# Kernel tuning notes

Measured on AMD Instinct MI355X. Metric: run time of the kernel, lower is better.

Reference implementation:

```python
import jax, jax.numpy as jnp
import numpy as np

HEADS = 16
DIM = 1024


def setup_inputs() -> dict:
    key = jax.random.key(0)
    ks = jax.random.split(key, 9)
    b, n, d = 2, 2048, DIM
    scale = 1.0 / np.sqrt(d)  # xavier-ish scale for weights
    x = jax.random.normal(ks[0], (b, n, d), dtype=jnp.float32)
    Wq = jax.random.normal(ks[1], (d, d), dtype=jnp.float32) * scale
    Wk = jax.random.normal(ks[2], (d, d), dtype=jnp.float32) * scale
    Wv = jax.random.normal(ks[3], (d, d), dtype=jnp.float32) * scale
    Wo = jax.random.normal(ks[4], (d, d), dtype=jnp.float32) * scale
    bq = jnp.zeros((d,), jnp.float32)
    bk = jnp.zeros((d,), jnp.float32)
    bv = jnp.zeros((d,), jnp.float32)
    bo = jnp.zeros((d,), jnp.float32)
    return {"x": x, "Wq": Wq, "bq": bq, "Wk": Wk, "bk": bk,
            "Wv": Wv, "bv": bv, "Wo": Wo, "bo": bo}


def reference(x, Wq, bq, Wk, bk, Wv, bv, Wo, bo):
    b, n, d = x.shape
    h = HEADS
    hd = d // h
    # torch Linear: y = x @ W.T + b  (W stored [out, in]; here square so W given as [d,d])
    q = x @ Wq.T + bq
    k = x @ Wk.T + bk
    v = x @ Wv.T + bv
    # b n (h d) -> b h n d
    q = q.reshape(b, n, h, hd).transpose(0, 2, 1, 3)
    k = k.reshape(b, n, h, hd).transpose(0, 2, 1, 3)
    v = v.reshape(b, n, h, hd).transpose(0, 2, 1, 3)
    # NOTE: scale is 1/sqrt(dim), not 1/sqrt(head_dim), faithful to source.
    scores = jnp.einsum('bhqd,bhkd->bhqk', q, k) / jnp.sqrt(jnp.float32(d))
    attn = jax.nn.softmax(scores, axis=-1)
    out = jnp.einsum('bhqk,bhkd->bhqd', attn, v)
    out = out.transpose(0, 2, 1, 3).reshape(b, n, d)  # b h n d -> b n (h d)
    return out @ Wo.T + bo
```

## Files before the change

### kernel.cpp

```cpp
#include <hip/hip_runtime.h>

typedef unsigned short u16t;
typedef __attribute__((ext_vector_type(8))) short bf16x8;
typedef __attribute__((ext_vector_type(4))) float f32x4;

#define DM   1024
#define SEQL 2048
#define NHD  16
#define HDD  64

#define GLL16(g, l) __builtin_amdgcn_global_load_lds( \
    (const __attribute__((address_space(1))) void*)(g), \
    (__attribute__((address_space(3))) void*)(l), 16, 0, 0)

__device__ __forceinline__ u16t f2bf(float f) {
  unsigned u = __float_as_uint(f);
  return (u16t)((u + 0x7fffu + ((u >> 16) & 1u)) >> 16);
}
__device__ __forceinline__ unsigned pack_bf16_2(float a, float b) {
  const unsigned ua = __float_as_uint(a) + 0x8000u;
  const unsigned ub = __float_as_uint(b) + 0x8000u;
  return __builtin_amdgcn_perm(ub, ua, 0x07060302);
}

struct ConvArgs { const float* src[5]; u16t* dst[5]; };

__global__ __launch_bounds__(256) void conv_kernel(ConvArgs a) {
  const int gid = blockIdx.x * 256 + threadIdx.x;
  const int e = gid << 2;
  int sel, off;
  if (e < 4194304) { sel = 0; off = e; }
  else { const int r = e - 4194304; sel = 1 + (r >> 20); off = r & 1048575; }
  const float4 f = *(const float4*)(a.src[sel] + off);
  union { u16t s[4]; uint2 u; } o;
  o.s[0] = f2bf(f.x); o.s[1] = f2bf(f.y); o.s[2] = f2bf(f.z); o.s[3] = f2bf(f.w);
  *(uint2*)(a.dst[sel] + off) = o.u;
}

__device__ __forceinline__ int gslot(int m, int kc) { return (m << 2) + (kc ^ ((m >> 1) & 3)); }

template<int MODE>
__device__ __forceinline__ void qkv_body(
    const u16t* __restrict__ X, const u16t* __restrict__ W,
    const float* __restrict__ bias, float oscale, u16t* __restrict__ outB,
    u16t* As, u16t* Bs, u16t* Es)
{
  const int tid = threadIdx.x;
  const int l = tid & 63, w = tid >> 6, q = l >> 4, ln = l & 15;
  const int trow0 = blockIdx.y << 7;
  const int dcol0 = blockIdx.x << 7;
  const int wm = (w >> 1) << 6, wn = (w & 1) << 6;

  const int s0 = (w << 6) + l, s1 = s0 + 256;
  const int m0 = s0 >> 2, kc0 = (s0 & 3) ^ ((m0 >> 1) & 3);
  const int m1 = s1 >> 2, kc1 = (s1 & 3) ^ ((m1 >> 1) & 3);
  const u16t* gA0 = X + (size_t)(trow0 + m0) * DM + (kc0 << 3);
  const u16t* gA1 = X + (size_t)(trow0 + m1) * DM + (kc1 << 3);
  const u16t* gB0 = W + (size_t)(dcol0 + m0) * DM + (kc0 << 3);
  const u16t* gB1 = W + (size_t)(dcol0 + m1) * DM + (kc1 << 3);
  u16t* const lA0 = &As[(w << 6) << 3];
  u16t* const lA1 = &As[((w << 6) + 256) << 3];
  u16t* const lB0 = &Bs[(w << 6) << 3];
  u16t* const lB1 = &Bs[((w << 6) + 256) << 3];

  f32x4 acc[4][4] = {};

  for (int kt = 0; kt < DM; kt += 32) {
    __syncthreads();
    GLL16(gA0 + kt, lA0);
    GLL16(gA1 + kt, lA1);
    GLL16(gB0 + kt, lB0);
    GLL16(gB1 + kt, lB1);
    __syncthreads();

    bf16x8 af[4], bfr[4];
    #pragma unroll
    for (int mi = 0; mi < 4; ++mi) {
      const int r = wm + (mi << 4) + ln;
      af[mi] = *(const bf16x8*)&((MODE == 1 ? Bs : As)[gslot(r, q) << 3]);
    }
    #pragma unroll
    for (int ni = 0; ni < 4; ++ni) {
      const int r = wn + (ni << 4) + ln;
      bfr[ni] = *(const bf16x8*)&((MODE == 1 ? As : Bs)[gslot(r, q) << 3]);
    }
    #pragma unroll
    for (int mi = 0; mi < 4; ++mi)
      #pragma unroll
      for (int ni = 0; ni < 4; ++ni)
        acc[mi][ni] = __builtin_amdgcn_mfma_f32_16x16x32_bf16(af[mi], bfr[ni], acc[mi][ni], 0, 0, 0);
  }

  __syncthreads();

  if (MODE == 1) {
    #pragma unroll
    for (int mi = 0; mi < 4; ++mi) {
      const int dl = wm + (mi << 4) + (q << 2);
      const float4 b4 = *(const float4*)&bias[dcol0 + dl];
      #pragma unroll
      for (int ni = 0; ni < 4; ++ni) {
        const int tl = wn + (ni << 4) + ln;
        uint2 pk;
        pk.x = pack_bf16_2((acc[mi][ni][0] + b4.x) * oscale, (acc[mi][ni][1] + b4.y) * oscale);
        pk.y = pack_bf16_2((acc[mi][ni][2] + b4.z) * oscale, (acc[mi][ni][3] + b4.w) * oscale);
        *(uint2*)&Es[tl * 136 + dl] = pk;
      }
    }
    __syncthreads();
    #pragma unroll
    for (int it = 0; it < 8; ++it) {
      const int u = (it << 8) + tid;
      const int tl = u >> 4, c8 = u & 15;
      const uint4 vv = *(const uint4*)&Es[tl * 136 + (c8 << 3)];
      const int tok = trow0 + tl;
      const int b = tok >> 11, n = tok & (SEQL - 1);
      const int dg = dcol0 + (c8 << 3);
      const int h = dg >> 6, hd = dg & 63;
      *(uint4*)&outB[((size_t)(b * NHD + h) * SEQL + n) * HDD + hd] = vv;
    }
  } else {
    #pragma unroll
    for (int ni = 0; ni < 4; ++ni) {
      const int dl = wn + (ni << 4) + ln;
      const float bv = bias[dcol0 + dl];
      #pragma unroll
      for (int mi = 0; mi < 4; ++mi) {
        const int g = (wm >> 2) + (mi << 2) + q;
        const int g6 = g & 15;
        const int gp = (g & 16) | (g6 & 8) | ((g6 & 3) << 1) | ((g6 >> 2) & 1);
        uint2 pk;
        pk.x = pack_bf16_2(acc[mi][ni][0] + bv, acc[mi][ni][1] + bv);
        pk.y = pack_bf16_2(acc[mi][ni][2] + bv, acc[mi][ni][3] + bv);
        *(uint2*)&Es[dl * 136 + (gp << 2)] = pk;
      }
    }
    __syncthreads();
    #pragma unroll
    for (int it = 0; it < 8; ++it) {
      const int u = (it << 8) + tid;
      const int dl = u >> 4, c8 = u & 15;
      const uint4 vv = *(const uint4*)&Es[dl * 136 + (c8 << 3)];
      const int dg = dcol0 + dl;
      const int h = dg >> 6, hd = dg & 63;
      const int b = trow0 >> 11;
      const int n = (trow0 & (SEQL - 1)) + (c8 << 3);
      *(uint4*)&outB[((size_t)(b * NHD + h) * HDD + hd) * SEQL + n] = vv;
    }
  }
}

struct QKVArgs { const u16t* W[3]; const float* b[3]; u16t* dst[3]; };

__global__ __launch_bounds__(256) void qkv_kernel(const u16t* __restrict__ X, QKVArgs g) {
  __shared__ alignas(16) u16t smem[17408];
  u16t* As = smem;
  u16t* Bs = smem + 4096;
  u16t* Es = smem;
  const int z = blockIdx.z;
  if (z == 2)      qkv_body<2>(X, g.W[2], g.b[2], 1.0f, g.dst[2], As, Bs, Es);
  else if (z == 1) qkv_body<1>(X, g.W[1], g.b[1], 1.0f, g.dst[1], As, Bs, Es);
  else             qkv_body<1>(X, g.W[0], g.b[0], 0.03125f, g.dst[0], As, Bs, Es);
}

__global__ __launch_bounds__(256) void outproj_kernel(
    const u16t* __restrict__ A, const u16t* __restrict__ W,
    const float* __restrict__ bias, float* __restrict__ outF)
{
  __shared__ alignas(16) u16t As[128 * 32];
  __shared__ alignas(16) u16t Bs[128 * 32];

  const int tid = threadIdx.x;
  const int l = tid & 63, w = tid >> 6, q = l >> 4, ln = l & 15;
  const int row0 = blockIdx.y << 7;
  const int col0 = blockIdx.x << 7;
  const int wm = (w >> 1) << 6, wn = (w & 1) << 6;

  const int s0 = (w << 6) + l, s1 = s0 + 256;
  const int m0 = s0 >> 2, kc0 = (s0 & 3) ^ ((m0 >> 1) & 3);
  const int m1 = s1 >> 2, kc1 = (s1 & 3) ^ ((m1 >> 1) & 3);
  const u16t* gA0 = A + (size_t)(row0 + m0) * DM + (kc0 << 3);
  const u16t* gA1 = A + (size_t)(row0 + m1) * DM + (kc1 << 3);
  const u16t* gB0 = W + (size_t)(col0 + m0) * DM + (kc0 << 3);
  const u16t* gB1 = W + (size_t)(col0 + m1) * DM + (kc1 << 3);
  u16t* const lA0 = &As[(w << 6) << 3];
  u16t* const lA1 = &As[((w << 6) + 256) << 3];
  u16t* const lB0 = &Bs[(w << 6) << 3];
  u16t* const lB1 = &Bs[((w << 6) + 256) << 3];

  f32x4 acc[4][4] = {};

  for (int kt = 0; kt < DM; kt += 32) {
    __syncthreads();
    GLL16(gA0 + kt, lA0);
    GLL16(gA1 + kt, lA1);
    GLL16(gB0 + kt, lB0);
    GLL16(gB1 + kt, lB1);
    __syncthreads();

    bf16x8 af[4], bfr[4];
    #pragma unroll
    for (int mi = 0; mi < 4; ++mi)
      af[mi] = *(const bf16x8*)&As[gslot(wm + (mi << 4) + ln, q) << 3];
    #pragma unroll
    for (int ni = 0; ni < 4; ++ni)
      bfr[ni] = *(const bf16x8*)&Bs[gslot(wn + (ni << 4) + ln, q) << 3];
    #pragma unroll
    for (int mi = 0; mi < 4; ++mi)
      #pragma unroll
      for (int ni = 0; ni < 4; ++ni)
        acc[mi][ni] = __builtin_amdgcn_mfma_f32_16x16x32_bf16(af[mi], bfr[ni], acc[mi][ni], 0, 0, 0);
  }

  #pragma unroll
  for (int ni = 0; ni < 4; ++ni) {
    const int col = col0 + wn + (ni << 4) + ln;
    const float bv = bias[col];
    #pragma unroll
    for (int mi = 0; mi < 4; ++mi)
      #pragma unroll
      for (int r = 0; r < 4; ++r) {
        const int row = row0 + wm + (mi << 4) + (q << 2) + r;
        outF[(size_t)row * DM + col] = acc[mi][ni][r] + bv;
      }
  }
}

__global__ __launch_bounds__(256) void attn_kernel(
    const u16t* __restrict__ Qb, const u16t* __restrict__ Kb,
    const u16t* __restrict__ Vt, u16t* __restrict__ ctx)
{
  __shared__ alignas(16) u16t smem[17408];
  u16t* Qs = smem;
  u16t* Os = smem;
  u16t* Ks = smem + 9216;
  u16t* Vs = smem + 13312;

  const int tid = threadIdx.x;
  const int l = tid & 63, w = tid >> 6;
  const int q = l >> 4, ln = l & 15;
  const int bh = blockIdx.y, q0 = blockIdx.x << 7;
  const size_t hb = (size_t)bh * SEQL * HDD;
  const u16t* Qg = Qb + hb;
  const u16t* Kg = Kb + hb;
  const u16t* Vg = Vt + hb;

  #pragma unroll
  for (int i = 0; i < 4; ++i) {
    const int u = (i << 8) + tid;
    const int r = u >> 3, c = (u & 7) ^ (r & 7);
    GLL16(Qg + (size_t)(q0 + r) * HDD + (c << 3), &Qs[((i << 8) + (w << 6)) << 3]);
  }

  f32x4 accO[2][4] = {};
  float lsum[2] = {0.f, 0.f};
  bf16x8 qf[2][2];

  for (int k0 = 0; k0 < SEQL; k0 += 64) {
    __syncthreads();
    #pragma unroll
    for (int i = 0; i < 2; ++i) {
      const int u = (i << 8) + tid;
      const int r = u >> 3, c = (u & 7) ^ (r & 7);
      GLL16(Kg + (size_t)(k0 + r) * HDD + (c << 3), &Ks[((i << 8) + (w << 6)) << 3]);
      GLL16(Vg + (size_t)r * SEQL + k0 + (c << 3), &Vs[((i << 8) + (w << 6)) << 3]);
    }
    __syncthreads();

    if (k0 == 0) {
      #pragma unroll
      for (int g = 0; g < 2; ++g) {
        const int qr = (w << 5) + (g << 4) + ln;
        #pragma unroll
        for (int ks = 0; ks < 2; ++ks) {
          const int hc = (ks << 2) + q;
          qf[g][ks] = *(const bf16x8*)&Qs[((qr << 3) + (hc ^ (qr & 7))) << 3];
        }
      }
    }

    f32x4 sc[2][4] = {{}, {}};
    #pragma unroll
    for (int ks = 0; ks < 2; ++ks) {
      const int hc = (ks << 2) + q;
      #pragma unroll
      for (int ni = 0; ni < 4; ++ni) {
        const int kr = (ni << 4) + ln;
        const bf16x8 ak = *(const bf16x8*)&Ks[((kr << 3) + (hc ^ (kr & 7))) << 3];
        #pragma unroll
        for (int g = 0; g < 2; ++g)
          sc[g][ni] = __builtin_amdgcn_mfma_f32_16x16x32_bf16(ak, qf[g][ks], sc[g][ni], 0, 0, 0);
      }
    }

    unsigned pk01[2][4], pk23[2][4];
    #pragma unroll
    for (int g = 0; g < 2; ++g) {
      float ps = 0.0f;
      #pragma unroll
      for (int ni = 0; ni < 4; ++ni) {
        const float p0 = __expf(sc[g][ni][0]);
        const float p1 = __expf(sc[g][ni][1]);
        const float p2 = __expf(sc[g][ni][2]);
        const float p3 = __expf(sc[g][ni][3]);
        ps += (p0 + p1) + (p2 + p3);
        pk01[g][ni] = pack_bf16_2(p0, p1);
        pk23[g][ni] = pack_bf16_2(p2, p3);
      }
      ps += __shfl_xor(ps, 16);
      ps += __shfl_xor(ps, 32);
      lsum[g] += ps;
    }

    #pragma unroll
    for (int ks = 0; ks < 2; ++ks) {
      union { unsigned u[4]; bf16x8 v; } bfv[2];
      #pragma unroll
      for (int g = 0; g < 2; ++g) {
        bfv[g].u[0] = pk01[g][(ks << 1) + 0];
        bfv[g].u[1] = pk23[g][(ks << 1) + 0];
        bfv[g].u[2] = pk01[g][(ks << 1) + 1];
        bfv[g].u[3] = pk23[g][(ks << 1) + 1];
      }
      const int c = (ks << 2) + q;
      #pragma unroll
      for (int nio = 0; nio < 4; ++nio) {
        const int vr = (nio << 4) + ln;
        const bf16x8 av = *(const bf16x8*)&Vs[((vr << 3) + (c ^ (vr & 7))) << 3];
        #pragma unroll
        for (int g = 0; g < 2; ++g)
          accO[g][nio] = __builtin_amdgcn_mfma_f32_16x16x32_bf16(av, bfv[g].v, accO[g][nio], 0, 0, 0);
      }
    }
  }

  #pragma unroll
  for (int g = 0; g < 2; ++g) {
    const float inv = 1.0f / lsum[g];
    const int tl = (w << 5) + (g << 4) + ln;
    #pragma unroll
    for (int nio = 0; nio < 4; ++nio) {
      uint2 pk;
      pk.x = pack_bf16_2(accO[g][nio][0] * inv, accO[g][nio][1] * inv);
      pk.y = pack_bf16_2(accO[g][nio][2] * inv, accO[g][nio][3] * inv);
      *(uint2*)&Os[tl * 72 + (nio << 4) + (q << 2)] = pk;
    }
  }
  __syncthreads();
  const int h = bh & (NHD - 1), bi = bh >> 4;
  #pragma unroll
  for (int it = 0; it < 4; ++it) {
    const int u = (it << 8) + tid;
    const int tl = u >> 3, c8 = u & 7;
    const uint4 vv = *(const uint4*)&Os[tl * 72 + (c8 << 3)];
    *(uint4*)&ctx[((size_t)(bi * SEQL + q0 + tl)) * DM + (h << 6) + (c8 << 3)] = vv;
  }
}

extern "C" void kernel_launch(void* const* d_in, const int* in_sizes, int n_in,
                              void* d_out, int out_size, void* d_ws, size_t ws_size,
                              hipStream_t stream)
{
  const float* x  = (const float*)d_in[0];
  const float* Wq = (const float*)d_in[1];
  const float* bq = (const float*)d_in[2];
  const float* Wk = (const float*)d_in[3];
  const float* bk = (const float*)d_in[4];
  const float* Wv = (const float*)d_in[5];
  const float* bv = (const float*)d_in[6];
  const float* Wo = (const float*)d_in[7];
  const float* bo = (const float*)d_in[8];
  float* out = (float*)d_out;

  u16t* p = (u16t*)d_ws;
  u16t* xb  = p;  p += 4194304;
  u16t* Wqb = p;  p += 1048576;
  u16t* Wkb = p;  p += 1048576;
  u16t* Wvb = p;  p += 1048576;
  u16t* Wob = p;  p += 1048576;
  u16t* Qbf = p;  p += 4194304;
  u16t* Kbf = p;  p += 4194304;
  u16t* Vtb = p;  p += 4194304;
  u16t* ctx = p;  p += 4194304;

  ConvArgs ca;
  ca.src[0] = x;  ca.dst[0] = xb;
  ca.src[1] = Wq; ca.dst[1] = Wqb;
  ca.src[2] = Wk; ca.dst[2] = Wkb;
  ca.src[3] = Wv; ca.dst[3] = Wvb;
  ca.src[4] = Wo; ca.dst[4] = Wob;
  conv_kernel<<<8192, 256, 0, stream>>>(ca);

  QKVArgs qa;
  qa.W[0] = Wqb; qa.W[1] = Wkb; qa.W[2] = Wvb;
  qa.b[0] = bq;  qa.b[1] = bk;  qa.b[2] = bv;
  qa.dst[0] = Qbf; qa.dst[1] = Kbf; qa.dst[2] = Vtb;
  qkv_kernel<<<dim3(8, 32, 3), 256, 0, stream>>>(xb, qa);

  attn_kernel<<<dim3(16, 32), 256, 0, stream>>>(Qbf, Kbf, Vtb, ctx);

  outproj_kernel<<<dim3(8, 32), 256, 0, stream>>>(ctx, Wob, bo, out);
}
```

Measured before the change: 206.2 us.

## Double-buffer LDS tiles in QKV, out-proj and attention loops

After: 192.7 us. 1.07x faster.

```diff
diff --git a/kernel.cpp b/kernel.cpp
--- a/kernel.cpp
+++ b/kernel.cpp
@@ -43,8 +43,10 @@
 __device__ __forceinline__ void qkv_body(
     const u16t* __restrict__ X, const u16t* __restrict__ W,
     const float* __restrict__ bias, float oscale, u16t* __restrict__ outB,
-    u16t* As, u16t* Bs, u16t* Es)
+    u16t* smem)
 {
+  u16t* const Es = smem;
+
   const int tid = threadIdx.x;
   const int l = tid & 63, w = tid >> 6, q = l >> 4, ln = l & 15;
   const int trow0 = blockIdx.y << 7;
@@ -58,31 +60,40 @@
   const u16t* gA1 = X + (size_t)(trow0 + m1) * DM + (kc1 << 3);
   const u16t* gB0 = W + (size_t)(dcol0 + m0) * DM + (kc0 << 3);
   const u16t* gB1 = W + (size_t)(dcol0 + m1) * DM + (kc1 << 3);
-  u16t* const lA0 = &As[(w << 6) << 3];
-  u16t* const lA1 = &As[((w << 6) + 256) << 3];
-  u16t* const lB0 = &Bs[(w << 6) << 3];
-  u16t* const lB1 = &Bs[((w << 6) + 256) << 3];
+  const int dO0 = (w << 6) << 3;
+  const int dO1 = ((w << 6) + 256) << 3;
 
   f32x4 acc[4][4] = {};
 
+  GLL16(gA0, smem + dO0);
+  GLL16(gA1, smem + dO1);
+  GLL16(gB0, smem + 4096 + dO0);
+  GLL16(gB1, smem + 4096 + dO1);
+
   for (int kt = 0; kt < DM; kt += 32) {
+    const int it = kt >> 5;
+    u16t* const curA = smem + ((it & 1) ? 8192 : 0);
+    u16t* const curB = curA + 4096;
     __syncthreads();
-    GLL16(gA0 + kt, lA0);
-    GLL16(gA1 + kt, lA1);
-    GLL16(gB0 + kt, lB0);
-    GLL16(gB1 + kt, lB1);
-    __syncthreads();
+    if (kt + 32 < DM) {
+      u16t* const nA = smem + ((it & 1) ? 0 : 8192);
+      u16t* const nB = nA + 4096;
+      GLL16(gA0 + kt + 32, nA + dO0);
+      GLL16(gA1 + kt + 32, nA + dO1);
+      GLL16(gB0 + kt + 32, nB + dO0);
+      GLL16(gB1 + kt + 32, nB + dO1);
+    }
 
     bf16x8 af[4], bfr[4];
     #pragma unroll
     for (int mi = 0; mi < 4; ++mi) {
       const int r = wm + (mi << 4) + ln;
-      af[mi] = *(const bf16x8*)&((MODE == 1 ? Bs : As)[gslot(r, q) << 3]);
+      af[mi] = *(const bf16x8*)&((MODE == 1 ? curB : curA)[gslot(r, q) << 3]);
     }
     #pragma unroll
     for (int ni = 0; ni < 4; ++ni) {
       const int r = wn + (ni << 4) + ln;
-      bfr[ni] = *(const bf16x8*)&((MODE == 1 ? As : Bs)[gslot(r, q) << 3]);
+      bfr[ni] = *(const bf16x8*)&((MODE == 1 ? curA : curB)[gslot(r, q) << 3]);
     }
     #pragma unroll
     for (int mi = 0; mi < 4; ++mi)
@@ -154,21 +165,17 @@
 
 __global__ __launch_bounds__(256) void qkv_kernel(const u16t* __restrict__ X, QKVArgs g) {
   __shared__ alignas(16) u16t smem[17408];
-  u16t* As = smem;
-  u16t* Bs = smem + 4096;
-  u16t* Es = smem;
   const int z = blockIdx.z;
-  if (z == 2)      qkv_body<2>(X, g.W[2], g.b[2], 1.0f, g.dst[2], As, Bs, Es);
-  else if (z == 1) qkv_body<1>(X, g.W[1], g.b[1], 1.0f, g.dst[1], As, Bs, Es);
-  else             qkv_body<1>(X, g.W[0], g.b[0], 0.03125f, g.dst[0], As, Bs, Es);
+  if (z == 2)      qkv_body<2>(X, g.W[2], g.b[2], 1.0f, g.dst[2], smem);
+  else if (z == 1) qkv_body<1>(X, g.W[1], g.b[1], 1.0f, g.dst[1], smem);
+  else             qkv_body<1>(X, g.W[0], g.b[0], 0.03125f, g.dst[0], smem);
 }
 
 __global__ __launch_bounds__(256) void outproj_kernel(
     const u16t* __restrict__ A, const u16t* __restrict__ W,
     const float* __restrict__ bias, float* __restrict__ outF)
 {
-  __shared__ alignas(16) u16t As[128 * 32];
-  __shared__ alignas(16) u16t Bs[128 * 32];
+  __shared__ alignas(16) u16t smem[16384];
 
   const int tid = threadIdx.x;
   const int l = tid & 63, w = tid >> 6, q = l >> 4, ln = l & 15;
@@ -183,28 +190,37 @@
   const u16t* gA1 = A + (size_t)(row0 + m1) * DM + (kc1 << 3);
   const u16t* gB0 = W + (size_t)(col0 + m0) * DM + (kc0 << 3);
   const u16t* gB1 = W + (size_t)(col0 + m1) * DM + (kc1 << 3);
-  u16t* const lA0 = &As[(w << 6) << 3];
-  u16t* const lA1 = &As[((w << 6) + 256) << 3];
-  u16t* const lB0 = &Bs[(w << 6) << 3];
-  u16t* const lB1 = &Bs[((w << 6) + 256) << 3];
+  const int dO0 = (w << 6) << 3;
+  const int dO1 = ((w << 6) + 256) << 3;
 
   f32x4 acc[4][4] = {};
 
+  GLL16(gA0, smem + dO0);
+  GLL16(gA1, smem + dO1);
+  GLL16(gB0, smem + 4096 + dO0);
+  GLL16(gB1, smem + 4096 + dO1);
+
   for (int kt = 0; kt < DM; kt += 32) {
+    const int it = kt >> 5;
+    u16t* const curA = smem + ((it & 1) ? 8192 : 0);
+    u16t* const curB = curA + 4096;
     __syncthreads();
-    GLL16(gA0 + kt, lA0);
-    GLL16(gA1 + kt, lA1);
-    GLL16(gB0 + kt, lB0);
-    GLL16(gB1 + kt, lB1);
-    __syncthreads();
+    if (kt + 32 < DM) {
+      u16t* const nA = smem + ((it & 1) ? 0 : 8192);
+      u16t* const nB = nA + 4096;
+      GLL16(gA0 + kt + 32, nA + dO0);
+      GLL16(gA1 + kt + 32, nA + dO1);
+      GLL16(gB0 + kt + 32, nB + dO0);
+      GLL16(gB1 + kt + 32, nB + dO1);
+    }
 
     bf16x8 af[4], bfr[4];
     #pragma unroll
     for (int mi = 0; mi < 4; ++mi)
-      af[mi] = *(const bf16x8*)&As[gslot(wm + (mi << 4) + ln, q) << 3];
+      af[mi] = *(const bf16x8*)&curA[gslot(wm + (mi << 4) + ln, q) << 3];
     #pragma unroll
     for (int ni = 0; ni < 4; ++ni)
-      bfr[ni] = *(const bf16x8*)&Bs[gslot(wn + (ni << 4) + ln, q) << 3];
+      bfr[ni] = *(const bf16x8*)&curB[gslot(wn + (ni << 4) + ln, q) << 3];
     #pragma unroll
     for (int mi = 0; mi < 4; ++mi)
       #pragma unroll
@@ -230,11 +246,9 @@
     const u16t* __restrict__ Qb, const u16t* __restrict__ Kb,
     const u16t* __restrict__ Vt, u16t* __restrict__ ctx)
 {
-  __shared__ alignas(16) u16t smem[17408];
-  u16t* Qs = smem;
-  u16t* Os = smem;
-  u16t* Ks = smem + 9216;
-  u16t* Vs = smem + 13312;
+  __shared__ alignas(16) u16t smem[25600];
+  u16t* const Qs = smem;
+  u16t* const Os = smem;
 
   const int tid = threadIdx.x;
   const int l = tid & 63, w = tid >> 6;
@@ -252,22 +266,40 @@
     GLL16(Qg + (size_t)(q0 + r) * HDD + (c << 3), &Qs[((i << 8) + (w << 6)) << 3]);
   }
 
+  const int u0 = tid,       r0 = u0 >> 3, c0 = (u0 & 7) ^ (r0 & 7);
+  const int u1 = 256 + tid, r1 = u1 >> 3, c1 = (u1 & 7) ^ (r1 & 7);
+  const u16t* const kS0 = Kg + (size_t)r0 * HDD + (c0 << 3);
+  const u16t* const kS1 = Kg + (size_t)r1 * HDD + (c1 << 3);
+  const u16t* const vS0 = Vg + (size_t)r0 * SEQL + (c0 << 3);
+  const u16t* const vS1 = Vg + (size_t)r1 * SEQL + (c1 << 3);
+  const int dK0 = (w << 6) << 3, dK1 = (256 + (w << 6)) << 3;
+
+  GLL16(kS0, smem + 9216 + dK0);
+  GLL16(kS1, smem + 9216 + dK1);
+  GLL16(vS0, smem + 13312 + dK0);
+  GLL16(vS1, smem + 13312 + dK1);
+
   f32x4 accO[2][4] = {};
   float lsum[2] = {0.f, 0.f};
   bf16x8 qf[2][2];
 
-  for (int k0 = 0; k0 < SEQL; k0 += 64) {
+  for (int t = 0; t < SEQL / 64; ++t) {
+    const int cb = (t & 1) ? 8192 : 0;
+    u16t* const Ks = smem + 9216 + cb;
+    u16t* const Vs = smem + 13312 + cb;
     __syncthreads();
-    #pragma unroll
-    for (int i = 0; i < 2; ++i) {
-      const int u = (i << 8) + tid;
-      const int r = u >> 3, c = (u & 7) ^ (r & 7);
-      GLL16(Kg + (size_t)(k0 + r) * HDD + (c << 3), &Ks[((i << 8) + (w << 6)) << 3]);
-      GLL16(Vg + (size_t)r * SEQL + k0 + (c << 3), &Vs[((i << 8) + (w << 6)) << 3]);
-    }
-    __syncthreads();
-
-    if (k0 == 0) {
+    if (t + 1 < SEQL / 64) {
+      const int nb = (t & 1) ? 0 : 8192;
+      u16t* const nK = smem + 9216 + nb;
+      u16t* const nV = smem + 13312 + nb;
+      const int ko = (t + 1) << 6;
+      GLL16(kS0 + (size_t)ko * HDD, nK + dK0);
+      GLL16(kS1 + (size_t)ko * HDD, nK + dK1);
+      GLL16(vS0 + ko, nV + dK0);
+      GLL16(vS1 + ko, nV + dK1);
+    }
+
+    if (t == 0) {
       #pragma unroll
       for (int g = 0; g < 2; ++g) {
         const int qr = (w << 5) + (g << 4) + ln;
@@ -334,6 +366,7 @@
     }
   }
 
+  __syncthreads();
   #pragma unroll
   for (int g = 0; g < 2; ++g) {
     const float inv = 1.0f / lsum[g];
```
